# Kernel optimization log

Measured on AMD Instinct MI355X. Metric: run time of the kernel, lower is better.

Reference implementation:

```python
import jax, jax.numpy as jnp
import numpy as np

B, NS, NT = 8, 1024, 1024
SRC, TGT, OUT, H = 1024, 1024, 1024, 8
DH = OUT // H  # per-head dim = 128


def setup_inputs() -> dict:
    key = jax.random.key(0)
    ks = jax.random.split(key, 9)
    s = 0.02
    return {
        "src": jax.random.normal(ks[0], (B, NS, SRC), jnp.float32),
        "tgt": jax.random.normal(ks[1], (B, NT, TGT), jnp.float32),
        "src_mask": jnp.ones((B, NS), jnp.float32),
        "tgt_mask": jnp.ones((B, NT), jnp.float32),
        "Ws": jax.random.normal(ks[2], (2 * OUT, SRC), jnp.float32) * s,
        "bs": jnp.zeros((2 * OUT,), jnp.float32),
        "Wt": jax.random.normal(ks[3], (OUT, TGT), jnp.float32) * s,
        "bt": jnp.zeros((OUT,), jnp.float32),
        "Wo": jax.random.normal(ks[4], (OUT, OUT + TGT), jnp.float32) * s,
        "bo": jnp.zeros((OUT,), jnp.float32),
    }


def reference(src, tgt, src_mask, tgt_mask, Ws, bs, Wt, bt, Wo, bo):
    # src_lin / tgt_lin (FCNet = linear, no activation, drop=0 at eval)
    src_trans = jnp.einsum("bsf,of->bso", src, Ws) + bs  # [B,NS,2*OUT]
    tgt_trans = jnp.einsum("btf,of->bto", tgt, Wt) + bt  # [B,NT,OUT]
    src_trans = src_trans * src_mask[:, :, None]
    tgt_trans = tgt_trans * tgt_mask[:, :, None]

    src_key, src_val = jnp.split(src_trans, 2, axis=2)  # each [B,NS,OUT]
    # head split along channels == reshape to [.., H, DH]
    k = src_key.reshape(B, NS, H, DH)
    v = src_val.reshape(B, NS, H, DH)
    q = tgt_trans.reshape(B, NT, H, DH)

    scores = jnp.einsum("bthd,bshd->bhts", q, k) / jnp.sqrt(jnp.float32(DH))
    scores = jnp.where(src_mask[:, None, None, :] == 0, -jnp.inf, scores)
    attn = jax.nn.softmax(scores, axis=-1)  # [B,H,NT,NS]
    tgt_update = jnp.einsum("bhts,bshd->bthd", attn, v).reshape(B, NT, OUT)

    cat_tgt = jnp.concatenate([tgt, tgt_update], axis=2)  # [B,NT,TGT+OUT]
    update_tgt = jnp.einsum("btf,of->bto", cat_tgt, Wo) + bo
    return update_tgt
```

## Files before the change

### kernel.cpp

```cpp
#include <hip/hip_runtime.h>


typedef __bf16 bf16x8 __attribute__((ext_vector_type(8)));
typedef float f32x4 __attribute__((ext_vector_type(4)));
typedef unsigned short u16;
typedef unsigned short u16x8 __attribute__((ext_vector_type(8)));

#define MFMA16(a, b, c) __builtin_amdgcn_mfma_f32_16x16x32_bf16((a), (b), (c), 0, 0, 0)

__device__ __forceinline__ float bf2f(u16 b) {
  return __uint_as_float(((unsigned)b) << 16);
}
__device__ __forceinline__ u16 f2bf(float f) {
  unsigned u = __float_as_uint(f);
  u += 0x7fffu + ((u >> 16) & 1u);
  return (u16)(u >> 16);
}
__device__ __forceinline__ u16 f2bf_hw(float f) {
  __bf16 h = (__bf16)f;
  return __builtin_bit_cast(u16, h);
}

__device__ __forceinline__ void async16(const u16* g, u16* l) {
  __builtin_amdgcn_global_load_lds(
      (const __attribute__((address_space(1))) unsigned int*)g,
      (__attribute__((address_space(3))) unsigned int*)l, 16, 0, 0);
}

struct Cvt5 {
  const float* src[5];
  unsigned cnt4[5];
  unsigned ooff[5];
};

__global__ __launch_bounds__(256)
void cvt5_kernel(Cvt5 a, u16* __restrict__ out, unsigned total4)
{
  unsigned gid = blockIdx.x * 256u + threadIdx.x;
  if (gid >= total4) return;
  unsigned rem = gid;
  int s = 0;
  while (s < 4 && rem >= a.cnt4[s]) { rem -= a.cnt4[s]; ++s; }
  const float4 v = ((const float4*)a.src[s])[rem];
  ushort4 o;
  o.x = f2bf(v.x); o.y = f2bf(v.y); o.z = f2bf(v.z); o.w = f2bf(v.w);
  *(ushort4*)(out + a.ooff[s] + (size_t)rem * 4) = o;
}

template <int MODE, typename OutT>
__global__ __launch_bounds__(256, 3)
void gemm_bt_kernel(const u16* __restrict__ A0, const u16* __restrict__ A1,
                    int splitK,
                    const u16* __restrict__ Bw, const float* __restrict__ bias,
                    const float* __restrict__ rowscale,
                    OutT* __restrict__ C, int N, int K)
{
  __shared__ u16 As[128 * 32];
  __shared__ u16 Bs[128 * 32];
  const int tid  = threadIdx.x;
  const int lane = tid & 63;
  const int w    = tid >> 6;
  const int wm = w >> 1, wn = w & 1;
  const int quad = lane >> 4, lr = lane & 15;
  const unsigned nwg  = gridDim.x * gridDim.y;
  const unsigned wgid = blockIdx.y * gridDim.x + blockIdx.x;
  const unsigned swz  = (wgid & 7u) * (nwg >> 3) + (wgid >> 3);
  const int m0 = (int)(swz / gridDim.x) * 128;
  const int n0 = (int)(swz % gridDim.x) * 128;

  const f32x4 z4 = {0.f, 0.f, 0.f, 0.f};
  f32x4 acc[4][4];
#pragma unroll
  for (int i = 0; i < 4; ++i)
#pragma unroll
    for (int j = 0; j < 4; ++j)
      acc[i][j] = z4;

  const int acol = (tid & 3) * 8;

  auto kstep = [&](const u16* Ap, int lda, int kk, int k0) {
    __syncthreads();
#pragma unroll
    for (int it = 0; it < 2; ++it) {
      const int row = it * 64 + (tid >> 2);
      const int ldsbase = (it * 256 + (tid & 192)) * 8;
      async16(Ap + (size_t)(m0 + row) * lda + (kk + acol), &As[ldsbase]);
      async16(Bw + (size_t)(n0 + row) * K   + (k0 + acol), &Bs[ldsbase]);
    }
    __syncthreads();

    bf16x8 af[4], bfr[4];
#pragma unroll
    for (int i = 0; i < 4; ++i)
      af[i] = *(const bf16x8*)&As[(wm * 64 + i * 16 + lr) * 32 + quad * 8];
#pragma unroll
    for (int j = 0; j < 4; ++j)
      bfr[j] = *(const bf16x8*)&Bs[(wn * 64 + j * 16 + lr) * 32 + quad * 8];
#pragma unroll
    for (int i = 0; i < 4; ++i)
#pragma unroll
      for (int j = 0; j < 4; ++j)
        acc[i][j] = MFMA16(af[i], bfr[j], acc[i][j]);
  };

  for (int k0 = 0; k0 < splitK; k0 += 32) kstep(A0, splitK, k0, k0);
  for (int k0 = splitK; k0 < K; k0 += 32) kstep(A1, K - splitK, k0 - splitK, k0);

  float bv[4];
#pragma unroll
  for (int j = 0; j < 4; ++j)
    bv[j] = bias[n0 + wn * 64 + j * 16 + lr];

  if constexpr (MODE == 0) {
#pragma unroll
    for (int i = 0; i < 4; ++i)
#pragma unroll
      for (int r = 0; r < 4; ++r) {
        const int grow = m0 + wm * 64 + i * 16 + quad * 4 + r;
        float rs = 1.f;
        if (rowscale) rs = rowscale[grow];
#pragma unroll
        for (int j = 0; j < 4; ++j) {
          const int gcol = n0 + wn * 64 + j * 16 + lr;
          C[(size_t)grow * N + gcol] = (OutT)((acc[i][j][r] + bv[j]) * rs);
        }
      }
  } else {
    __shared__ u16 kvtile[16384];
    const int bb  = m0 >> 10;
    const int s0b = m0 & 1023;
    const bool isK = (n0 < 1024);
    const int h = isK ? (n0 >> 7) : ((n0 - 1024) >> 7);
    const size_t bh = (size_t)(bb * 8 + h);

#pragma unroll
    for (int i = 0; i < 4; ++i)
#pragma unroll
      for (int r = 0; r < 4; ++r) {
        const int sl = wm * 64 + i * 16 + quad * 4 + r;
        float rs = 1.f;
        if (rowscale) rs = rowscale[m0 + sl];
#pragma unroll
        for (int j = 0; j < 4; ++j) {
          const int d = wn * 64 + j * 16 + lr;
          const float val = (acc[i][j][r] + bv[j]) * rs;
          int addr;
          if (isK) {
            addr = ((d >> 3) * 128 + sl) * 8 + (d & 7);
          } else {
            addr = (sl >> 6) * 8192 + (((sl >> 3) & 7) * 128 + d) * 8 + (sl & 7);
          }
          kvtile[addr] = f2bf(val);
        }
      }
    __syncthreads();

    const size_t gbase = isK
        ? (bh * 131072 + (size_t)s0b * 8)
        : ((size_t)8388608 + bh * 131072 + (size_t)(s0b >> 6) * 8192);
#pragma unroll
    for (int it = 0; it < 8; ++it) {
      const int idx = it * 256 + tid;
      size_t dst;
      if (isK) {
        const int dc = idx >> 7;
        dst = gbase + (size_t)dc * 8192 + (size_t)(idx & 127) * 8;
      } else {
        dst = gbase + (size_t)idx * 8;
      }
      *(u16x8*)((u16*)C + dst) = *(const u16x8*)&kvtile[idx * 8];
    }
  }
}

template <>
__global__ __launch_bounds__(256, 3)
void gemm_bt_kernel<0, u16>(const u16* __restrict__ A0, const u16* __restrict__ A1,
                            int splitK,
                            const u16* __restrict__ Bw, const float* __restrict__ bias,
                            const float* __restrict__ rowscale,
                            u16* __restrict__ C, int N, int K)
{
  __shared__ u16 As[128 * 32];
  __shared__ u16 Bs[128 * 32];
  const int tid  = threadIdx.x;
  const int lane = tid & 63;
  const int w    = tid >> 6;
  const int wm = w >> 1, wn = w & 1;
  const int quad = lane >> 4, lr = lane & 15;
  const unsigned nwg  = gridDim.x * gridDim.y;
  const unsigned wgid = blockIdx.y * gridDim.x + blockIdx.x;
  const unsigned swz  = (wgid & 7u) * (nwg >> 3) + (wgid >> 3);
  const int m0 = (int)(swz / gridDim.x) * 128;
  const int n0 = (int)(swz % gridDim.x) * 128;

  const f32x4 z4 = {0.f, 0.f, 0.f, 0.f};
  f32x4 acc[4][4];
#pragma unroll
  for (int i = 0; i < 4; ++i)
#pragma unroll
    for (int j = 0; j < 4; ++j)
      acc[i][j] = z4;

  const int acol = (tid & 3) * 8;

  auto kstep = [&](const u16* Ap, int lda, int kk, int k0) {
    __syncthreads();
#pragma unroll
    for (int it = 0; it < 2; ++it) {
      const int row = it * 64 + (tid >> 2);
      const int ldsbase = (it * 256 + (tid & 192)) * 8;
      async16(Ap + (size_t)(m0 + row) * lda + (kk + acol), &As[ldsbase]);
      async16(Bw + (size_t)(n0 + row) * K   + (k0 + acol), &Bs[ldsbase]);
    }
    __syncthreads();

    bf16x8 af[4], bfr[4];
#pragma unroll
    for (int i = 0; i < 4; ++i)
      af[i] = *(const bf16x8*)&As[(wm * 64 + i * 16 + lr) * 32 + quad * 8];
#pragma unroll
    for (int j = 0; j < 4; ++j)
      bfr[j] = *(const bf16x8*)&Bs[(wn * 64 + j * 16 + lr) * 32 + quad * 8];
#pragma unroll
    for (int i = 0; i < 4; ++i)
#pragma unroll
      for (int j = 0; j < 4; ++j)
        acc[i][j] = MFMA16(af[i], bfr[j], acc[i][j]);
  };

  for (int k0 = 0; k0 < splitK; k0 += 32) kstep(A0, splitK, k0, k0);
  for (int k0 = splitK; k0 < K; k0 += 32) kstep(A1, K - splitK, k0 - splitK, k0);

  float bv[4];
#pragma unroll
  for (int j = 0; j < 4; ++j)
    bv[j] = bias[n0 + wn * 64 + j * 16 + lr];

#pragma unroll
  for (int i = 0; i < 4; ++i)
#pragma unroll
    for (int r = 0; r < 4; ++r) {
      const int grow = m0 + wm * 64 + i * 16 + quad * 4 + r;
      float rs = 1.f;
      if (rowscale) rs = rowscale[grow];
#pragma unroll
      for (int j = 0; j < 4; ++j) {
        const int gcol = n0 + wn * 64 + j * 16 + lr;
        C[(size_t)grow * N + gcol] = f2bf((acc[i][j][r] + bv[j]) * rs);
      }
    }
}

#define SCLOG2E 0.12751813754618667f

__global__ __launch_bounds__(256, 2)
void flash_kernel(const u16* __restrict__ q, const u16* __restrict__ Kg,
                  const u16* __restrict__ Vg,
                  const float* __restrict__ smask, u16* __restrict__ upd)
{
  __shared__ u16 Ks[64 * 128];
  __shared__ u16 Vs[64 * 128];
  __shared__ u16 Ps[4][2 * 16 * 64];

  const int tid  = threadIdx.x;
  const int lane = tid & 63;
  const int w    = tid >> 6;
  const int quad = lane >> 4, lr = lane & 15;
  const int bh_i = blockIdx.x;
  const int qt   = blockIdx.y;
  const int b = bh_i >> 3, h = bh_i & 7;
  const size_t bh = (size_t)bh_i;

  const size_t qrow0 = (size_t)b * 1024 + qt * 128 + w * 16;

  bf16x8 qf[2][4];
#pragma unroll
  for (int s = 0; s < 2; ++s)
#pragma unroll
    for (int kk = 0; kk < 4; ++kk)
      qf[s][kk] = *(const bf16x8*)
          &q[(qrow0 + s * 64 + lr) * 1024 + h * 128 + kk * 32 + quad * 8];

  const f32x4 z4 = {0.f, 0.f, 0.f, 0.f};
  f32x4 oacc[2][8];
#pragma unroll
  for (int s = 0; s < 2; ++s)
#pragma unroll
    for (int jd = 0; jd < 8; ++jd) oacc[s][jd] = z4;
  float lsum[2][4] = {{0.f, 0.f, 0.f, 0.f}, {0.f, 0.f, 0.f, 0.f}};

  for (int s0 = 0; s0 < 1024; s0 += 64) {
    const int t = s0 >> 6;
    __syncthreads();
#pragma unroll
    for (int it = 0; it < 4; ++it) {
      const int dc = it * 4 + w;
      async16(Kg + (((bh * 16 + dc) * 1024) + s0 + lane) * 8,
              &Ks[(it * 256 + (tid & 192)) * 8]);
    }
#pragma unroll
    for (int it = 0; it < 4; ++it) {
      const int f = it * 256 + tid;
      async16(Vg + ((bh * 16 + t) * 1024 + f) * 8,
              &Vs[(it * 256 + (tid & 192)) * 8]);
    }
    __syncthreads();

    f32x4 sacc[2][4];
#pragma unroll
    for (int s = 0; s < 2; ++s)
#pragma unroll
      for (int j = 0; j < 4; ++j) sacc[s][j] = z4;
    __builtin_amdgcn_s_setprio(1);
#pragma unroll
    for (int kk = 0; kk < 4; ++kk) {
      bf16x8 kb[4];
#pragma unroll
      for (int j = 0; j < 4; ++j)
        kb[j] = *(const bf16x8*)&Ks[((kk * 4 + quad) * 64 + j * 16 + lr) * 8];
#pragma unroll
      for (int s = 0; s < 2; ++s)
#pragma unroll
        for (int j = 0; j < 4; ++j)
          sacc[s][j] = MFMA16(qf[s][kk], kb[j], sacc[s][j]);
    }
    __builtin_amdgcn_s_setprio(0);

    float mb[4];
#pragma unroll
    for (int j = 0; j < 4; ++j) {
      const float mv = smask[b * 1024 + s0 + j * 16 + lr];
      mb[j] = (mv == 0.f) ? -1e30f : 0.f;
    }

#pragma unroll
    for (int s = 0; s < 2; ++s)
#pragma unroll
      for (int r = 0; r < 4; ++r) {
        const int row = quad * 4 + r;
        const int rsw = (row & 7) * 8;
        float ps = 0.f;
#pragma unroll
        for (int j = 0; j < 4; ++j) {
          const float p = exp2f(fmaf(sacc[s][j][r], SCLOG2E, mb[j]));
          ps += p;
          Ps[w][s * 1024 + row * 64 + ((j * 16 + lr) ^ rsw)] = f2bf_hw(p);
        }
        lsum[s][r] += ps;
      }

    __builtin_amdgcn_s_setprio(1);
#pragma unroll
    for (int kk2 = 0; kk2 < 2; ++kk2) {
      bf16x8 pa[2], vb[8];
#pragma unroll
      for (int s = 0; s < 2; ++s)
        pa[s] = *(const bf16x8*)
            &Ps[w][s * 1024 + lr * 64 + ((kk2 * 32 + quad * 8) ^ ((lr & 7) * 8))];
#pragma unroll
      for (int jd = 0; jd < 8; ++jd)
        vb[jd] = *(const bf16x8*)&Vs[((kk2 * 4 + quad) * 128 + jd * 16 + lr) * 8];
#pragma unroll
      for (int s = 0; s < 2; ++s)
#pragma unroll
        for (int jd = 0; jd < 8; ++jd)
          oacc[s][jd] = MFMA16(pa[s], vb[jd], oacc[s][jd]);
    }
    __builtin_amdgcn_s_setprio(0);
  }

#pragma unroll
  for (int s = 0; s < 2; ++s)
#pragma unroll
    for (int r = 0; r < 4; ++r) {
      float l = lsum[s][r];
      l += __shfl_xor(l, 1);
      l += __shfl_xor(l, 2);
      l += __shfl_xor(l, 4);
      l += __shfl_xor(l, 8);
      const float inv = 1.f / l;
      const size_t grow = qrow0 + s * 64 + quad * 4 + r;
#pragma unroll
      for (int jd = 0; jd < 8; ++jd)
        upd[grow * 1024 + h * 128 + jd * 16 + lr] = f2bf_hw(oacc[s][jd][r] * inv);
    }
}

__global__ void magic_kernel(float* out, float val)
{
  if (threadIdx.x == 0 && blockIdx.x == 0) out[0] = val;
}

extern "C" void kernel_launch(void* const* d_in, const int* in_sizes, int n_in,
                              void* d_out, int out_size, void* d_ws, size_t ws_size,
                              hipStream_t stream)
{
  static const int dict_sz[10]   = {8388608, 8388608, 8192, 8192, 2097152,
                                    2048, 1048576, 1024, 2097152, 1024};
  static const int sorted_sz[10] = {2097152, 2097152, 1048576, 1024, 2048,
                                    1024, 8388608, 8192, 8388608, 8192};
  bool is_dict = (n_in == 10), is_sorted = (n_in == 10);
  if (n_in == 10) {
    for (int i = 0; i < 10; ++i) {
      if (in_sizes[i] != dict_sz[i])   is_dict = false;
      if (in_sizes[i] != sorted_sz[i]) is_sorted = false;
    }
  }

  const float *src, *tgt, *smask, *tmask, *Ws, *bs, *Wt, *bt, *Wo, *bo;
  if (is_sorted) {
    Wo    = (const float*)d_in[0];
    Ws    = (const float*)d_in[1];
    Wt    = (const float*)d_in[2];
    bo    = (const float*)d_in[3];
    bs    = (const float*)d_in[4];
    bt    = (const float*)d_in[5];
    src   = (const float*)d_in[6];
    smask = (const float*)d_in[7];
    tgt   = (const float*)d_in[8];
    tmask = (const float*)d_in[9];
  } else {
    src   = (const float*)d_in[0];
    tgt   = (const float*)d_in[1];
    smask = (const float*)d_in[2];
    tmask = (const float*)d_in[3];
    Ws    = (const float*)d_in[4];
    bs    = (const float*)d_in[5];
    Wt    = (const float*)d_in[6];
    bt    = (const float*)d_in[7];
    Wo    = (const float*)d_in[8];
    bo    = (const float*)d_in[9];
  }
  float* out = (float*)d_out;

  const size_t KV = 16777216, Q = 8388608, UPD = 8388608;
  const unsigned segsz[5] = {8388608u, 8388608u, 2097152u, 1048576u, 2097152u};
  size_t total_u16 = KV + Q + UPD;
  unsigned aoff[5], off = 0, total4 = 0;
  for (int i = 0; i < 5; ++i) {
    aoff[i] = off;
    off += segsz[i];
    total4 += segsz[i] / 4u;
  }
  total_u16 += off;

  unsigned ws_mb = (unsigned)(ws_size >> 20);
  if (ws_mb > 999u) ws_mb = 999u;
  if (!is_dict && !is_sorted) {
    magic_kernel<<<dim3(1), dim3(64), 0, stream>>>(out, 4000.f + (float)ws_mb);
    return;
  }
  if (ws_size < total_u16 * 2) {
    magic_kernel<<<dim3(1), dim3(64), 0, stream>>>(out, 3000.f + (float)ws_mb);
    return;
  }

  u16* kvbuf  = (u16*)d_ws;
  u16* qbuf   = kvbuf + KV;
  u16* updbuf = qbuf + Q;
  u16* arena  = updbuf + UPD;

  Cvt5 ca;
  const float* segp[5] = {src, tgt, Ws, Wt, Wo};
  for (int i = 0; i < 5; ++i) {
    ca.src[i]  = segp[i];
    ca.cnt4[i] = segsz[i] / 4u;
    ca.ooff[i] = aoff[i];
  }
  const u16* srcb = arena + aoff[0];
  const u16* tgtb = arena + aoff[1];
  const u16* Wsb  = arena + aoff[2];
  const u16* Wtb  = arena + aoff[3];
  const u16* Wob  = arena + aoff[4];

  dim3 blk(256);
  cvt5_kernel<<<dim3((total4 + 255u) / 256u), blk, 0, stream>>>(ca, arena, total4);
  gemm_bt_kernel<1, u16><<<dim3(16, 64), blk, 0, stream>>>(
      srcb, nullptr, 1024, Wsb, bs, smask, kvbuf, 2048, 1024);
  gemm_bt_kernel<0, u16><<<dim3(8, 64), blk, 0, stream>>>(
      tgtb, nullptr, 1024, Wtb, bt, tmask, qbuf, 1024, 1024);
  flash_kernel<<<dim3(64, 8), blk, 0, stream>>>(
      qbuf, kvbuf, kvbuf + 8388608, smask, updbuf);
  gemm_bt_kernel<0, float><<<dim3(8, 64), blk, 0, stream>>>(
      tgtb, updbuf, 1024, Wob, bo, nullptr, out, 1024, 2048);
}
```

Before: 317.7 us.

## Merge K/V and Q projection GEMMs into one launch with swizzled LDS epilogue

Combines the src K/V projection and the tgt Q projection into a single grid (24x64 tiles). Each tile picks its A operand, weights, bias and mask by column range, which removes one launch and its tail underutilisation. It also XOR-swizzles the LDS staging tile used for the head-major K/V scatter to cut bank conflicts, and switches to hardware bf16 conversion. The output GEMM is specialised with constant strides and no rowscale branch. The added per-tile branch is a uniform selection.

```diff
diff --git a/kernel.cpp b/kernel.cpp
--- a/kernel.cpp
+++ b/kernel.cpp
@@ -47,13 +47,148 @@
   *(ushort4*)(out + a.ooff[s] + (size_t)rem * 4) = o;
 }
 
-template <int MODE, typename OutT>
 __global__ __launch_bounds__(256, 3)
-void gemm_bt_kernel(const u16* __restrict__ A0, const u16* __restrict__ A1,
-                    int splitK,
-                    const u16* __restrict__ Bw, const float* __restrict__ bias,
-                    const float* __restrict__ rowscale,
-                    OutT* __restrict__ C, int N, int K)
+void gemm12_kernel(const u16* __restrict__ srcb, const u16* __restrict__ tgtb,
+                   const u16* __restrict__ Wsb, const u16* __restrict__ Wtb,
+                   const float* __restrict__ bs, const float* __restrict__ bt,
+                   const float* __restrict__ smask, const float* __restrict__ tmask,
+                   u16* __restrict__ kvbuf, u16* __restrict__ qbuf)
+{
+  __shared__ u16 As[128 * 32];
+  __shared__ u16 Bs[128 * 32];
+  __shared__ u16 kvtile[16384];
+
+  const int tid  = threadIdx.x;
+  const int lane = tid & 63;
+  const int w    = tid >> 6;
+  const int wm = w >> 1, wn = w & 1;
+  const int quad = lane >> 4, lr = lane & 15;
+
+  const unsigned nwg  = gridDim.x * gridDim.y;
+  const unsigned wgid = blockIdx.y * gridDim.x + blockIdx.x;
+  const unsigned swz  = (wgid & 7u) * (nwg >> 3) + (wgid >> 3);
+  const int nt = (int)(swz % gridDim.x);
+  const int mt = (int)(swz / gridDim.x);
+  const int m0 = mt * 128;
+  const int n0 = nt * 128;
+
+  const bool isQ = (n0 >= 2048);
+  const u16* Ap = isQ ? tgtb : srcb;
+  const u16* Bp = isQ ? (Wtb + (size_t)(n0 - 2048) * 1024)
+                      : (Wsb + (size_t)n0 * 1024);
+  const float* bias = isQ ? (bt + (n0 - 2048)) : (bs + n0);
+  const float* rsc  = isQ ? tmask : smask;
+
+  const f32x4 z4 = {0.f, 0.f, 0.f, 0.f};
+  f32x4 acc[4][4];
+#pragma unroll
+  for (int i = 0; i < 4; ++i)
+#pragma unroll
+    for (int j = 0; j < 4; ++j)
+      acc[i][j] = z4;
+
+  const int acol = (tid & 3) * 8;
+
+  for (int k0 = 0; k0 < 1024; k0 += 32) {
+    __syncthreads();
+#pragma unroll
+    for (int it = 0; it < 2; ++it) {
+      const int row = it * 64 + (tid >> 2);
+      const int ldsbase = (it * 256 + (tid & 192)) * 8;
+      async16(Ap + (size_t)(m0 + row) * 1024 + (k0 + acol), &As[ldsbase]);
+      async16(Bp + (size_t)row * 1024        + (k0 + acol), &Bs[ldsbase]);
+    }
+    __syncthreads();
+
+    bf16x8 af[4], bfr[4];
+#pragma unroll
+    for (int i = 0; i < 4; ++i)
+      af[i] = *(const bf16x8*)&As[(wm * 64 + i * 16 + lr) * 32 + quad * 8];
+#pragma unroll
+    for (int j = 0; j < 4; ++j)
+      bfr[j] = *(const bf16x8*)&Bs[(wn * 64 + j * 16 + lr) * 32 + quad * 8];
+#pragma unroll
+    for (int i = 0; i < 4; ++i)
+#pragma unroll
+      for (int j = 0; j < 4; ++j)
+        acc[i][j] = MFMA16(af[i], bfr[j], acc[i][j]);
+  }
+
+  float bv[4];
+#pragma unroll
+  for (int j = 0; j < 4; ++j)
+    bv[j] = bias[wn * 64 + j * 16 + lr];
+
+  if (isQ) {
+    const int c0 = n0 - 2048;
+#pragma unroll
+    for (int i = 0; i < 4; ++i)
+#pragma unroll
+      for (int r = 0; r < 4; ++r) {
+        const int grow = m0 + wm * 64 + i * 16 + quad * 4 + r;
+        const float rs = rsc[grow];
+#pragma unroll
+        for (int j = 0; j < 4; ++j) {
+          const int gcol = c0 + wn * 64 + j * 16 + lr;
+          qbuf[(size_t)grow * 1024 + gcol] = f2bf_hw((acc[i][j][r] + bv[j]) * rs);
+        }
+      }
+  } else {
+    const int bb  = m0 >> 10;
+    const int s0b = m0 & 1023;
+    const bool isK = (n0 < 1024);
+    const int h = (isK ? n0 : n0 - 1024) >> 7;
+    const size_t bh = (size_t)(bb * 8 + h);
+
+#pragma unroll
+    for (int i = 0; i < 4; ++i)
+#pragma unroll
+      for (int r = 0; r < 4; ++r) {
+        const int sl = wm * 64 + i * 16 + quad * 4 + r;
+        const float rs = rsc[m0 + sl];
+#pragma unroll
+        for (int j = 0; j < 4; ++j) {
+          const int d = wn * 64 + j * 16 + lr;
+          const float val = (acc[i][j][r] + bv[j]) * rs;
+          int c, e;
+          if (isK) {
+            c = (d >> 3) * 128 + sl;
+            c ^= ((c >> 2) & 2) ^ ((c >> 7) & 1);
+            e = d & 7;
+          } else {
+            c = (sl >> 6) * 1024 + (((sl >> 3) & 7) * 128) + d;
+            c ^= (c >> 7) & 1;
+            e = sl & 7;
+          }
+          kvtile[c * 8 + e] = f2bf_hw(val);
+        }
+      }
+    __syncthreads();
+
+    const size_t gbase = isK
+        ? (bh * 131072 + (size_t)s0b * 8)
+        : ((size_t)8388608 + bh * 131072 + (size_t)(s0b >> 6) * 8192);
+#pragma unroll
+    for (int it = 0; it < 8; ++it) {
+      const int idx = it * 256 + tid;
+      int lc;
+      size_t dst;
+      if (isK) {
+        lc  = idx ^ ((idx >> 2) & 2) ^ ((idx >> 7) & 1);
+        dst = gbase + (size_t)(idx >> 7) * 8192 + (size_t)(idx & 127) * 8;
+      } else {
+        lc  = idx ^ ((idx >> 7) & 1);
+        dst = gbase + (size_t)idx * 8;
+      }
+      *(u16x8*)(kvbuf + dst) = *(const u16x8*)&kvtile[lc * 8];
+    }
+  }
+}
+
+__global__ __launch_bounds__(256, 3)
+void gemm3_kernel(const u16* __restrict__ A0, const u16* __restrict__ A1,
+                  const u16* __restrict__ Bw, const float* __restrict__ bias,
+                  float* __restrict__ C)
 {
   __shared__ u16 As[128 * 32];
   __shared__ u16 Bs[128 * 32];
@@ -78,14 +213,14 @@
 
   const int acol = (tid & 3) * 8;
 
-  auto kstep = [&](const u16* Ap, int lda, int kk, int k0) {
+  auto kstep = [&](const u16* Ap, int kk, int k0) {
     __syncthreads();
 #pragma unroll
     for (int it = 0; it < 2; ++it) {
       const int row = it * 64 + (tid >> 2);
       const int ldsbase = (it * 256 + (tid & 192)) * 8;
-      async16(Ap + (size_t)(m0 + row) * lda + (kk + acol), &As[ldsbase]);
-      async16(Bw + (size_t)(n0 + row) * K   + (k0 + acol), &Bs[ldsbase]);
+      async16(Ap + (size_t)(m0 + row) * 1024 + (kk + acol), &As[ldsbase]);
+      async16(Bw + (size_t)(n0 + row) * 2048 + (k0 + acol), &Bs[ldsbase]);
     }
     __syncthreads();
 
@@ -103,151 +238,23 @@
         acc[i][j] = MFMA16(af[i], bfr[j], acc[i][j]);
   };
 
-  for (int k0 = 0; k0 < splitK; k0 += 32) kstep(A0, splitK, k0, k0);
-  for (int k0 = splitK; k0 < K; k0 += 32) kstep(A1, K - splitK, k0 - splitK, k0);
+  for (int k0 = 0; k0 < 1024; k0 += 32) kstep(A0, k0, k0);
+  for (int k0 = 1024; k0 < 2048; k0 += 32) kstep(A1, k0 - 1024, k0);
 
   float bv[4];
 #pragma unroll
   for (int j = 0; j < 4; ++j)
     bv[j] = bias[n0 + wn * 64 + j * 16 + lr];
 
-  if constexpr (MODE == 0) {
-#pragma unroll
-    for (int i = 0; i < 4; ++i)
-#pragma unroll
-      for (int r = 0; r < 4; ++r) {
-        const int grow = m0 + wm * 64 + i * 16 + quad * 4 + r;
-        float rs = 1.f;
-        if (rowscale) rs = rowscale[grow];
-#pragma unroll
-        for (int j = 0; j < 4; ++j) {
-          const int gcol = n0 + wn * 64 + j * 16 + lr;
-          C[(size_t)grow * N + gcol] = (OutT)((acc[i][j][r] + bv[j]) * rs);
-        }
-      }
-  } else {
-    __shared__ u16 kvtile[16384];
-    const int bb  = m0 >> 10;
-    const int s0b = m0 & 1023;
-    const bool isK = (n0 < 1024);
-    const int h = isK ? (n0 >> 7) : ((n0 - 1024) >> 7);
-    const size_t bh = (size_t)(bb * 8 + h);
-
-#pragma unroll
-    for (int i = 0; i < 4; ++i)
-#pragma unroll
-      for (int r = 0; r < 4; ++r) {
-        const int sl = wm * 64 + i * 16 + quad * 4 + r;
-        float rs = 1.f;
-        if (rowscale) rs = rowscale[m0 + sl];
-#pragma unroll
-        for (int j = 0; j < 4; ++j) {
-          const int d = wn * 64 + j * 16 + lr;
-          const float val = (acc[i][j][r] + bv[j]) * rs;
-          int addr;
-          if (isK) {
-            addr = ((d >> 3) * 128 + sl) * 8 + (d & 7);
-          } else {
-            addr = (sl >> 6) * 8192 + (((sl >> 3) & 7) * 128 + d) * 8 + (sl & 7);
-          }
-          kvtile[addr] = f2bf(val);
-        }
-      }
-    __syncthreads();
-
-    const size_t gbase = isK
-        ? (bh * 131072 + (size_t)s0b * 8)
-        : ((size_t)8388608 + bh * 131072 + (size_t)(s0b >> 6) * 8192);
-#pragma unroll
-    for (int it = 0; it < 8; ++it) {
-      const int idx = it * 256 + tid;
-      size_t dst;
-      if (isK) {
-        const int dc = idx >> 7;
-        dst = gbase + (size_t)dc * 8192 + (size_t)(idx & 127) * 8;
-      } else {
-        dst = gbase + (size_t)idx * 8;
-      }
-      *(u16x8*)((u16*)C + dst) = *(const u16x8*)&kvtile[idx * 8];
-    }
-  }
-}
-
-template <>
-__global__ __launch_bounds__(256, 3)
-void gemm_bt_kernel<0, u16>(const u16* __restrict__ A0, const u16* __restrict__ A1,
-                            int splitK,
-                            const u16* __restrict__ Bw, const float* __restrict__ bias,
-                            const float* __restrict__ rowscale,
-                            u16* __restrict__ C, int N, int K)
-{
-  __shared__ u16 As[128 * 32];
-  __shared__ u16 Bs[128 * 32];
-  const int tid  = threadIdx.x;
-  const int lane = tid & 63;
-  const int w    = tid >> 6;
-  const int wm = w >> 1, wn = w & 1;
-  const int quad = lane >> 4, lr = lane & 15;
-  const unsigned nwg  = gridDim.x * gridDim.y;
-  const unsigned wgid = blockIdx.y * gridDim.x + blockIdx.x;
-  const unsigned swz  = (wgid & 7u) * (nwg >> 3) + (wgid >> 3);
-  const int m0 = (int)(swz / gridDim.x) * 128;
-  const int n0 = (int)(swz % gridDim.x) * 128;
-
-  const f32x4 z4 = {0.f, 0.f, 0.f, 0.f};
-  f32x4 acc[4][4];
-#pragma unroll
-  for (int i = 0; i < 4; ++i)
-#pragma unroll
-    for (int j = 0; j < 4; ++j)
-      acc[i][j] = z4;
-
-  const int acol = (tid & 3) * 8;
-
-  auto kstep = [&](const u16* Ap, int lda, int kk, int k0) {
-    __syncthreads();
-#pragma unroll
-    for (int it = 0; it < 2; ++it) {
-      const int row = it * 64 + (tid >> 2);
-      const int ldsbase = (it * 256 + (tid & 192)) * 8;
-      async16(Ap + (size_t)(m0 + row) * lda + (kk + acol), &As[ldsbase]);
-      async16(Bw + (size_t)(n0 + row) * K   + (k0 + acol), &Bs[ldsbase]);
-    }
-    __syncthreads();
-
-    bf16x8 af[4], bfr[4];
-#pragma unroll
-    for (int i = 0; i < 4; ++i)
-      af[i] = *(const bf16x8*)&As[(wm * 64 + i * 16 + lr) * 32 + quad * 8];
-#pragma unroll
-    for (int j = 0; j < 4; ++j)
-      bfr[j] = *(const bf16x8*)&Bs[(wn * 64 + j * 16 + lr) * 32 + quad * 8];
-#pragma unroll
-    for (int i = 0; i < 4; ++i)
-#pragma unroll
-      for (int j = 0; j < 4; ++j)
-        acc[i][j] = MFMA16(af[i], bfr[j], acc[i][j]);
-  };
-
-  for (int k0 = 0; k0 < splitK; k0 += 32) kstep(A0, splitK, k0, k0);
-  for (int k0 = splitK; k0 < K; k0 += 32) kstep(A1, K - splitK, k0 - splitK, k0);
-
-  float bv[4];
-#pragma unroll
-  for (int j = 0; j < 4; ++j)
-    bv[j] = bias[n0 + wn * 64 + j * 16 + lr];
-
 #pragma unroll
   for (int i = 0; i < 4; ++i)
 #pragma unroll
     for (int r = 0; r < 4; ++r) {
       const int grow = m0 + wm * 64 + i * 16 + quad * 4 + r;
-      float rs = 1.f;
-      if (rowscale) rs = rowscale[grow];
 #pragma unroll
       for (int j = 0; j < 4; ++j) {
         const int gcol = n0 + wn * 64 + j * 16 + lr;
-        C[(size_t)grow * N + gcol] = f2bf((acc[i][j][r] + bv[j]) * rs);
+        C[(size_t)grow * 1024 + gcol] = acc[i][j][r] + bv[j];
       }
     }
 }
@@ -476,12 +483,10 @@
 
   dim3 blk(256);
   cvt5_kernel<<<dim3((total4 + 255u) / 256u), blk, 0, stream>>>(ca, arena, total4);
-  gemm_bt_kernel<1, u16><<<dim3(16, 64), blk, 0, stream>>>(
-      srcb, nullptr, 1024, Wsb, bs, smask, kvbuf, 2048, 1024);
-  gemm_bt_kernel<0, u16><<<dim3(8, 64), blk, 0, stream>>>(
-      tgtb, nullptr, 1024, Wtb, bt, tmask, qbuf, 1024, 1024);
+  gemm12_kernel<<<dim3(24, 64), blk, 0, stream>>>(
+      srcb, tgtb, Wsb, Wtb, bs, bt, smask, tmask, kvbuf, qbuf);
   flash_kernel<<<dim3(64, 8), blk, 0, stream>>>(
       qbuf, kvbuf, kvbuf + 8388608, smask, updbuf);
-  gemm_bt_kernel<0, float><<<dim3(8, 64), blk, 0, stream>>>(
-      tgtb, updbuf, 1024, Wob, bo, nullptr, out, 1024, 2048);
-}
+  gemm3_kernel<<<dim3(8, 64), blk, 0, stream>>>(
+      tgtb, updbuf, Wob, bo, out);
+}
```

Measured after the change: 303.7 us. 1.05x faster.
